# Optimization experiments

Measured on AMD Instinct MI355X. Metric: run time of the kernel, lower is better.

Reference implementation:

```python
import jax, jax.numpy as jnp
import numpy as np


def setup_inputs() -> dict:
    key = jax.random.key(0)
    k1, k2 = jax.random.split(key)
    x = jax.random.normal(k1, (16, 8192, 128), dtype=jnp.float32)
    embed = jax.random.normal(k2, (1024, 128), dtype=jnp.float32)
    return {"x": x, "embed": embed}


def reference(x, embed):
    # preprocess: flatten leading dims -> (N, d)
    shape = x.shape
    xf = x.reshape(-1, shape[-1])  # (N, d)
    # quantize: negative squared Euclidean distance, argmax over codebook
    dist = (2.0 * (xf @ embed.T)
            - jnp.sum(xf * xf, axis=1, keepdims=True)
            - jnp.sum(embed * embed, axis=1)[None, :])
    embed_ind = jnp.argmax(dist, axis=-1)  # (N,)
    # postprocess indices back to input leading shape
    embed_ind = embed_ind.reshape(shape[:-1])
    # dequantize: embedding lookup
    quantize = embed[embed_ind]  # (..., d)
    return embed_ind, quantize
```

## Files before the change

### kernel.cpp

```cpp
#include <hip/hip_runtime.h>
#include <math.h>


typedef __attribute__((ext_vector_type(8)))  short short8_t;
typedef __attribute__((ext_vector_type(16))) float floatx16;

constexpr int D        = 128;
constexpr int KCODES   = 1024;
constexpr int NTILES   = 32;
constexpr int ROWS_BLK = 128;
constexpr float TAU    = 0.015f;

constexpr size_t WS_NCSQ = 0;
constexpr size_t WS_EHI  = 4096;
constexpr size_t WS_ELO  = WS_EHI + 262144;
constexpr size_t WS_EMBT = WS_ELO + 262144;

#define GLOBAL_AS __attribute__((address_space(1)))
#define LDS_AS    __attribute__((address_space(3)))

__device__ inline unsigned short bf16_rne(float v, float* back) {
    unsigned u = __float_as_uint(v);
    unsigned r = (u + 0x7FFFu + ((u >> 16) & 1u)) >> 16;
    *back = __uint_as_float(r << 16);
    return (unsigned short)r;
}

__global__ __launch_bounds__(256)
void ecb_prep(const float* __restrict__ embed, float* __restrict__ ncsq,
              unsigned short* __restrict__ ehi, unsigned short* __restrict__ elo,
              float* __restrict__ embT) {
    const int tid = threadIdx.x;
    const int cc = tid & 15;
    const int nl = tid >> 4;
    const int n  = blockIdx.x * 16 + nl;
    const int t = n >> 5, nn = n & 31;
    const float* src = embed + (size_t)n * D + cc * 8;
    float4 a = *(const float4*)src;
    float4 b = *(const float4*)(src + 4);
    float vv[8] = {a.x, a.y, a.z, a.w, b.x, b.y, b.z, b.w};
    float ss = 0.f;
    unsigned short hq[8], lq[8];
#pragma unroll
    for (int j = 0; j < 8; ++j) {
        ss = fmaf(vv[j], vv[j], ss);
        float hb, db;
        hq[j] = bf16_rne(vv[j], &hb);
        lq[j] = bf16_rne(vv[j] - hb, &db);
    }
    uint4 ph, pl;
    ph.x = (unsigned)hq[0] | ((unsigned)hq[1] << 16);
    ph.y = (unsigned)hq[2] | ((unsigned)hq[3] << 16);
    ph.z = (unsigned)hq[4] | ((unsigned)hq[5] << 16);
    ph.w = (unsigned)hq[6] | ((unsigned)hq[7] << 16);
    pl.x = (unsigned)lq[0] | ((unsigned)lq[1] << 16);
    pl.y = (unsigned)lq[2] | ((unsigned)lq[3] << 16);
    pl.z = (unsigned)lq[4] | ((unsigned)lq[5] << 16);
    pl.w = (unsigned)lq[6] | ((unsigned)lq[7] << 16);
    size_t dst = ((size_t)(t * 8 + (cc >> 1)) * 64 + (size_t)((cc & 1) * 32 + nn)) * 8;
    *(uint4*)(ehi + dst) = ph;
    *(uint4*)(elo + dst) = pl;
#pragma unroll
    for (int j = 0; j < 8; ++j) embT[(size_t)(cc * 8 + j) * KCODES + n] = vv[j];
#pragma unroll
    for (int m = 1; m < 16; m <<= 1) ss += __shfl_xor(ss, m, 64);
    if (cc == 0) ncsq[n] = -ss;
}

__global__ __launch_bounds__(256, 3)
void ecb_main(const float* __restrict__ x,
              const unsigned short* __restrict__ ehi, const unsigned short* __restrict__ elo,
              const float* __restrict__ ncsq, const float* __restrict__ embed,
              const float* __restrict__ embT,
              float* __restrict__ out_idx, float* __restrict__ out_q) {
    __shared__ short8_t ebuf[2][2][512];
    __shared__ float ncsq_s[KCODES];
    __shared__ int   sidx[ROWS_BLK];
    __shared__ unsigned char llist[ROWS_BLK];
    __shared__ unsigned lcount;

    const int tid  = threadIdx.x;
    const int lane = tid & 63, wave = tid >> 6;
    const int col  = lane & 31, h = lane >> 5;
    const long rowblk = (long)blockIdx.x * ROWS_BLK;
    const int  roww   = wave * 32;

    if (tid == 0) lcount = 0u;
    ((float4*)ncsq_s)[tid] = ((const float4*)ncsq)[tid];

    short8_t ah[8], al[8];
    {
        const float* xr = x + (rowblk + roww + col) * (long)D + h * 8;
#pragma unroll
        for (int c = 0; c < 8; ++c) {
            float4 a  = *(const float4*)(xr + c * 16);
            float4 b  = *(const float4*)(xr + c * 16 + 4);
            float vv[8] = {a.x, a.y, a.z, a.w, b.x, b.y, b.z, b.w};
            short8_t fh, fl;
#pragma unroll
            for (int j = 0; j < 8; ++j) {
                float v2x = vv[j] + vv[j];
                float hb, db;
                fh[j] = (short)bf16_rne(v2x, &hb);
                fl[j] = (short)bf16_rne(v2x - hb, &db);
            }
            ah[c] = fh;
            al[c] = fl;
        }
    }

    auto stage = [&](int t, int bb) {
        const char* gh = (const char*)ehi + (size_t)t * 8192;
        const char* gl = (const char*)elo + (size_t)t * 8192;
        char* lh = (char*)&ebuf[bb][0][0];
        char* ll = (char*)&ebuf[bb][1][0];
        const int off = wave * 2048;
        __builtin_amdgcn_global_load_lds((const GLOBAL_AS unsigned int*)(gh + off + lane * 16),
                                         (LDS_AS unsigned int*)(lh + off), 16, 0, 0);
        __builtin_amdgcn_global_load_lds((const GLOBAL_AS unsigned int*)(gh + off + 1024 + lane * 16),
                                         (LDS_AS unsigned int*)(lh + off + 1024), 16, 0, 0);
        __builtin_amdgcn_global_load_lds((const GLOBAL_AS unsigned int*)(gl + off + lane * 16),
                                         (LDS_AS unsigned int*)(ll + off), 16, 0, 0);
        __builtin_amdgcn_global_load_lds((const GLOBAL_AS unsigned int*)(gl + off + 1024 + lane * 16),
                                         (LDS_AS unsigned int*)(ll + off + 1024), 16, 0, 0);
    };

    float v1[16], v2[16];
#pragma unroll
    for (int j = 0; j < 16; ++j) { v1[j] = -INFINITY; v2[j] = -INFINITY; }

    __syncthreads();
    stage(0, 0);

#pragma unroll 1
    for (int t = 0; t < NTILES; ++t) {
        const int b = t & 1;
        if (t + 1 < NTILES) {
            stage(t + 1, b ^ 1);
            asm volatile("s_waitcnt vmcnt(4)" ::: "memory");
        } else {
            asm volatile("s_waitcnt vmcnt(0)" ::: "memory");
        }
        __builtin_amdgcn_sched_barrier(0);
        __builtin_amdgcn_s_barrier();

        const float negcs = ncsq_s[t * 32 + col];
        floatx16 accA, accB;
#pragma unroll
        for (int i = 0; i < 16; ++i) { accA[i] = negcs; accB[i] = 0.f; }

        __builtin_amdgcn_s_setprio(1);
#pragma unroll
        for (int s = 0; s < 8; ++s) {
            short8_t bh = ebuf[b][0][s * 64 + lane];
            short8_t bl = ebuf[b][1][s * 64 + lane];
            accA = __builtin_amdgcn_mfma_f32_32x32x16_bf16(ah[s], bh, accA, 0, 0, 0);
            accB = __builtin_amdgcn_mfma_f32_32x32x16_bf16(al[s], bh, accB, 0, 0, 0);
            accB = __builtin_amdgcn_mfma_f32_32x32x16_bf16(ah[s], bl, accB, 0, 0, 0);
        }
        __builtin_amdgcn_s_setprio(0);

#pragma unroll
        for (int j = 0; j < 16; ++j) {
            float sc = accA[j] + accB[j];
            unsigned u = (__float_as_uint(sc) & ~31u) | (unsigned)t;
            float cand = __uint_as_float(u);
            float mn = fminf(v1[j], cand);
            v1[j] = fmaxf(v1[j], cand);
            v2[j] = fmaxf(v2[j], mn);
        }

        asm volatile("s_waitcnt lgkmcnt(0)" ::: "memory");
        __builtin_amdgcn_sched_barrier(0);
        __builtin_amdgcn_s_barrier();
    }

#pragma unroll
    for (int j = 0; j < 16; ++j) {
        float a1 = v1[j], a2 = v2[j];
        int   c1 = (int)((__float_as_uint(a1) & 31u) << 5) | col;
#pragma unroll
        for (int m = 1; m < 32; m <<= 1) {
            float o1 = __shfl_xor(a1, m, 64);
            int   oc = __shfl_xor(c1, m, 64);
            float o2 = __shfl_xor(a2, m, 64);
            float lo = fminf(a1, o1);
            if (o1 > a1) { a1 = o1; c1 = oc; }
            a2 = fmaxf(fmaxf(a2, o2), lo);
        }
        if (col == j) {
            int row_local = roww + (j & 3) + 8 * (j >> 2) + 4 * h;
            sidx[row_local] = c1;
            out_idx[rowblk + row_local] = (float)c1;
            if (a1 - a2 < TAU) {
                unsigned p = atomicAdd(&lcount, 1u);
                llist[p] = (unsigned char)row_local;
            }
        }
    }
    __syncthreads();

    for (int i = tid; i < ROWS_BLK * 32; i += 256) {
        int r = i >> 5, q = i & 31;
        int code = sidx[r];
        float4 ev = *(const float4*)(embed + (size_t)code * D + q * 4);
        *(float4*)(out_q + (rowblk + r) * (long)D + q * 4) = ev;
    }
    __syncthreads();

    float* xs = (float*)&ebuf[0][0][0];
    float* bv = xs + D;
    int*   bi = (int*)(bv + 256);
    const unsigned nf = lcount;
    const float4* eT = (const float4*)embT;
    for (unsigned f = 0; f < nf; ++f) {
        const int rl  = llist[f];
        const long row = rowblk + rl;
        if (tid < 32) *(float4*)&xs[tid * 4] = *(const float4*)(x + row * D + tid * 4);
        __syncthreads();
        float4 dot = {0.f, 0.f, 0.f, 0.f};
#pragma unroll 8
        for (int k = 0; k < D; ++k) {
            float xv = xs[k];
            float4 e = eT[(size_t)k * 256 + tid];
            dot.x = fmaf(xv, e.x, dot.x);
            dot.y = fmaf(xv, e.y, dot.y);
            dot.z = fmaf(xv, e.z, dot.z);
            dot.w = fmaf(xv, e.w, dot.w);
        }
        const int c0 = tid * 4;
        float scs[4] = {fmaf(2.f, dot.x, ncsq_s[c0]),
                        fmaf(2.f, dot.y, ncsq_s[c0 + 1]),
                        fmaf(2.f, dot.z, ncsq_s[c0 + 2]),
                        fmaf(2.f, dot.w, ncsq_s[c0 + 3])};
        float best = -INFINITY; int bidx = 0;
#pragma unroll
        for (int i = 0; i < 4; ++i)
            if (scs[i] > best) { best = scs[i]; bidx = c0 + i; }
        bv[tid] = best; bi[tid] = bidx;
        __syncthreads();
        for (int s = 128; s > 0; s >>= 1) {
            if (tid < s) {
                float ov = bv[tid + s]; int oi = bi[tid + s];
                if (ov > bv[tid] || (ov == bv[tid] && oi < bi[tid])) { bv[tid] = ov; bi[tid] = oi; }
            }
            __syncthreads();
        }
        const int win = bi[0];
        if (tid == 0) out_idx[row] = (float)win;
        if (tid < 32) {
            float4 ev = *(const float4*)(embed + (size_t)win * D + tid * 4);
            *(float4*)(out_q + row * D + tid * 4) = ev;
        }
        __syncthreads();
    }
}

extern "C" void kernel_launch(void* const* d_in, const int* in_sizes, int n_in,
                              void* d_out, int out_size, void* d_ws, size_t ws_size,
                              hipStream_t stream) {
    const float* x     = (const float*)d_in[0];
    const float* embed = (const float*)d_in[1];
    const int N = in_sizes[0] / D;
    char* ws = (char*)d_ws;
    float*          ncsq = (float*)(ws + WS_NCSQ);
    unsigned short* ehi  = (unsigned short*)(ws + WS_EHI);
    unsigned short* elo  = (unsigned short*)(ws + WS_ELO);
    float*          embT = (float*)(ws + WS_EMBT);
    float* out_idx = (float*)d_out;
    float* out_q   = out_idx + N;

    hipLaunchKernelGGL(ecb_prep, dim3(64), dim3(256), 0, stream,
                       embed, ncsq, ehi, elo, embT);
    hipLaunchKernelGGL(ecb_main, dim3(N / ROWS_BLK), dim3(256), 0, stream,
                       x, ehi, elo, ncsq, embed, embT, out_idx, out_q);
}
```

Baseline: 239.2 us.

## Process two 32-row groups per wave to reuse each codebook tile

Each wave now handles 64 rows (two 32-row MFMA groups), so every block covers 256 rows and each codebook tile staged in LDS serves twice as many MFMAs. The correction MFMAs accumulate into a single accumulator per group, removing the separate accB and the final add. The first tile's prefetch is issued before the x loads so the two overlap. In exchange the extra A fragments and running top-2 state raise register pressure, occupancy drops to 2 blocks per SM, and there are half as many blocks.

```diff
diff --git a/kernel.cpp b/kernel.cpp
--- a/kernel.cpp
+++ b/kernel.cpp
@@ -8,7 +8,7 @@
 constexpr int D        = 128;
 constexpr int KCODES   = 1024;
 constexpr int NTILES   = 32;
-constexpr int ROWS_BLK = 128;
+constexpr int ROWS_BLK = 256;
 constexpr float TAU    = 0.015f;
 
 constexpr size_t WS_NCSQ = 0;
@@ -24,6 +24,20 @@
     unsigned r = (u + 0x7FFFu + ((u >> 16) & 1u)) >> 16;
     *back = __uint_as_float(r << 16);
     return (unsigned short)r;
+}
+
+__device__ inline void cvt8x2(const float4 a, const float4 b,
+                              short8_t* fh, short8_t* fl) {
+    float vv[8] = {a.x, a.y, a.z, a.w, b.x, b.y, b.z, b.w};
+    short8_t h, l;
+#pragma unroll
+    for (int j = 0; j < 8; ++j) {
+        float v2x = vv[j] + vv[j];
+        float hb, db;
+        h[j] = (short)bf16_rne(v2x, &hb);
+        l[j] = (short)bf16_rne(v2x - hb, &db);
+    }
+    *fh = h; *fl = l;
 }
 
 __global__ __launch_bounds__(256)
@@ -67,7 +81,7 @@
     if (cc == 0) ncsq[n] = -ss;
 }
 
-__global__ __launch_bounds__(256, 3)
+__global__ __launch_bounds__(256, 2)
 void ecb_main(const float* __restrict__ x,
               const unsigned short* __restrict__ ehi, const unsigned short* __restrict__ elo,
               const float* __restrict__ ncsq, const float* __restrict__ embed,
@@ -83,31 +97,9 @@
     const int lane = tid & 63, wave = tid >> 6;
     const int col  = lane & 31, h = lane >> 5;
     const long rowblk = (long)blockIdx.x * ROWS_BLK;
-    const int  roww   = wave * 32;
+    const int  roww   = wave * 64;
 
     if (tid == 0) lcount = 0u;
-    ((float4*)ncsq_s)[tid] = ((const float4*)ncsq)[tid];
-
-    short8_t ah[8], al[8];
-    {
-        const float* xr = x + (rowblk + roww + col) * (long)D + h * 8;
-#pragma unroll
-        for (int c = 0; c < 8; ++c) {
-            float4 a  = *(const float4*)(xr + c * 16);
-            float4 b  = *(const float4*)(xr + c * 16 + 4);
-            float vv[8] = {a.x, a.y, a.z, a.w, b.x, b.y, b.z, b.w};
-            short8_t fh, fl;
-#pragma unroll
-            for (int j = 0; j < 8; ++j) {
-                float v2x = vv[j] + vv[j];
-                float hb, db;
-                fh[j] = (short)bf16_rne(v2x, &hb);
-                fl[j] = (short)bf16_rne(v2x - hb, &db);
-            }
-            ah[c] = fh;
-            al[c] = fl;
-        }
-    }
 
     auto stage = [&](int t, int bb) {
         const char* gh = (const char*)ehi + (size_t)t * 8192;
@@ -125,12 +117,32 @@
                                          (LDS_AS unsigned int*)(ll + off + 1024), 16, 0, 0);
     };
 
-    float v1[16], v2[16];
-#pragma unroll
-    for (int j = 0; j < 16; ++j) { v1[j] = -INFINITY; v2[j] = -INFINITY; }
-
-    __syncthreads();
     stage(0, 0);
+    ((float4*)ncsq_s)[tid] = ((const float4*)ncsq)[tid];
+
+    short8_t ah0[8], al0[8], ah1[8], al1[8];
+    {
+        const float* xr0 = x + (rowblk + roww + col) * (long)D + h * 8;
+        const float* xr1 = xr0 + 32 * (long)D;
+#pragma unroll
+        for (int c = 0; c < 8; ++c) {
+            cvt8x2(*(const float4*)(xr0 + c * 16), *(const float4*)(xr0 + c * 16 + 4),
+                   &ah0[c], &al0[c]);
+            cvt8x2(*(const float4*)(xr1 + c * 16), *(const float4*)(xr1 + c * 16 + 4),
+                   &ah1[c], &al1[c]);
+        }
+    }
+
+    float v1a[16], v2a[16], v1b[16], v2b[16];
+#pragma unroll
+    for (int j = 0; j < 16; ++j) {
+        v1a[j] = -INFINITY; v2a[j] = -INFINITY;
+        v1b[j] = -INFINITY; v2b[j] = -INFINITY;
+    }
+
+    asm volatile("s_waitcnt lgkmcnt(0)" ::: "memory");
+    __builtin_amdgcn_sched_barrier(0);
+    __builtin_amdgcn_s_barrier();
 
 #pragma unroll 1
     for (int t = 0; t < NTILES; ++t) {
@@ -145,29 +157,36 @@
         __builtin_amdgcn_s_barrier();
 
         const float negcs = ncsq_s[t * 32 + col];
-        floatx16 accA, accB;
-#pragma unroll
-        for (int i = 0; i < 16; ++i) { accA[i] = negcs; accB[i] = 0.f; }
+        floatx16 acc0, acc1;
+#pragma unroll
+        for (int i = 0; i < 16; ++i) { acc0[i] = negcs; acc1[i] = negcs; }
 
         __builtin_amdgcn_s_setprio(1);
 #pragma unroll
         for (int s = 0; s < 8; ++s) {
             short8_t bh = ebuf[b][0][s * 64 + lane];
             short8_t bl = ebuf[b][1][s * 64 + lane];
-            accA = __builtin_amdgcn_mfma_f32_32x32x16_bf16(ah[s], bh, accA, 0, 0, 0);
-            accB = __builtin_amdgcn_mfma_f32_32x32x16_bf16(al[s], bh, accB, 0, 0, 0);
-            accB = __builtin_amdgcn_mfma_f32_32x32x16_bf16(ah[s], bl, accB, 0, 0, 0);
+            acc0 = __builtin_amdgcn_mfma_f32_32x32x16_bf16(ah0[s], bl, acc0, 0, 0, 0);
+            acc1 = __builtin_amdgcn_mfma_f32_32x32x16_bf16(ah1[s], bl, acc1, 0, 0, 0);
+            acc0 = __builtin_amdgcn_mfma_f32_32x32x16_bf16(al0[s], bh, acc0, 0, 0, 0);
+            acc1 = __builtin_amdgcn_mfma_f32_32x32x16_bf16(al1[s], bh, acc1, 0, 0, 0);
+            acc0 = __builtin_amdgcn_mfma_f32_32x32x16_bf16(ah0[s], bh, acc0, 0, 0, 0);
+            acc1 = __builtin_amdgcn_mfma_f32_32x32x16_bf16(ah1[s], bh, acc1, 0, 0, 0);
         }
         __builtin_amdgcn_s_setprio(0);
 
 #pragma unroll
         for (int j = 0; j < 16; ++j) {
-            float sc = accA[j] + accB[j];
-            unsigned u = (__float_as_uint(sc) & ~31u) | (unsigned)t;
-            float cand = __uint_as_float(u);
-            float mn = fminf(v1[j], cand);
-            v1[j] = fmaxf(v1[j], cand);
-            v2[j] = fmaxf(v2[j], mn);
+            unsigned u0 = (__float_as_uint(acc0[j]) & ~31u) | (unsigned)t;
+            float cand0 = __uint_as_float(u0);
+            float mn0 = fminf(v1a[j], cand0);
+            v1a[j] = fmaxf(v1a[j], cand0);
+            v2a[j] = fmaxf(v2a[j], mn0);
+            unsigned u1 = (__float_as_uint(acc1[j]) & ~31u) | (unsigned)t;
+            float cand1 = __uint_as_float(u1);
+            float mn1 = fminf(v1b[j], cand1);
+            v1b[j] = fmaxf(v1b[j], cand1);
+            v2b[j] = fmaxf(v2b[j], mn1);
         }
 
         asm volatile("s_waitcnt lgkmcnt(0)" ::: "memory");
@@ -175,29 +194,33 @@
         __builtin_amdgcn_s_barrier();
     }
 
-#pragma unroll
-    for (int j = 0; j < 16; ++j) {
-        float a1 = v1[j], a2 = v2[j];
-        int   c1 = (int)((__float_as_uint(a1) & 31u) << 5) | col;
-#pragma unroll
-        for (int m = 1; m < 32; m <<= 1) {
-            float o1 = __shfl_xor(a1, m, 64);
-            int   oc = __shfl_xor(c1, m, 64);
-            float o2 = __shfl_xor(a2, m, 64);
-            float lo = fminf(a1, o1);
-            if (o1 > a1) { a1 = o1; c1 = oc; }
-            a2 = fmaxf(fmaxf(a2, o2), lo);
-        }
-        if (col == j) {
-            int row_local = roww + (j & 3) + 8 * (j >> 2) + 4 * h;
-            sidx[row_local] = c1;
-            out_idx[rowblk + row_local] = (float)c1;
-            if (a1 - a2 < TAU) {
-                unsigned p = atomicAdd(&lcount, 1u);
-                llist[p] = (unsigned char)row_local;
+    auto merge_group = [&](float* v1, float* v2, int gbase) {
+#pragma unroll
+        for (int j = 0; j < 16; ++j) {
+            float a1 = v1[j], a2 = v2[j];
+            int   c1 = (int)((__float_as_uint(a1) & 31u) << 5) | col;
+#pragma unroll
+            for (int m = 1; m < 32; m <<= 1) {
+                float o1 = __shfl_xor(a1, m, 64);
+                int   oc = __shfl_xor(c1, m, 64);
+                float o2 = __shfl_xor(a2, m, 64);
+                float lo = fminf(a1, o1);
+                if (o1 > a1) { a1 = o1; c1 = oc; }
+                a2 = fmaxf(fmaxf(a2, o2), lo);
             }
-        }
-    }
+            if (col == j) {
+                int row_local = gbase + (j & 3) + 8 * (j >> 2) + 4 * h;
+                sidx[row_local] = c1;
+                out_idx[rowblk + row_local] = (float)c1;
+                if (a1 - a2 < TAU) {
+                    unsigned p = atomicAdd(&lcount, 1u);
+                    llist[p] = (unsigned char)row_local;
+                }
+            }
+        }
+    };
+    merge_group(v1a, v2a, roww);
+    merge_group(v1b, v2b, roww + 32);
     __syncthreads();
 
     for (int i = tid; i < ROWS_BLK * 32; i += 256) {
```

Measured after the change: 257.6 us. +7.7%, slower.

## Drop codebook low-bf16 split, triple-buffer tiles, widen fp32 refinement threshold

Applied to the files above, without the earlier changes.

The codebook is now held only as high bf16 (no low residual), so each tile needs two MFMAs instead of three and loads half the codebook data. Staging moves to a three-slot LDS ring with a single barrier per tile, and the runner-up tracking uses fmed3. The margin threshold for exact fp32 re-checking rises from 0.015 to 0.25 to cover the larger bf16 error. More rows may now fall into the serial fp32 refinement path, and the occupancy hint drops from 3 to 2 blocks.

```diff
diff --git a/kernel.cpp b/kernel.cpp
--- a/kernel.cpp
+++ b/kernel.cpp
@@ -9,12 +9,11 @@
 constexpr int KCODES   = 1024;
 constexpr int NTILES   = 32;
 constexpr int ROWS_BLK = 128;
-constexpr float TAU    = 0.015f;
+constexpr float TAU    = 0.25f;
 
 constexpr size_t WS_NCSQ = 0;
 constexpr size_t WS_EHI  = 4096;
-constexpr size_t WS_ELO  = WS_EHI + 262144;
-constexpr size_t WS_EMBT = WS_ELO + 262144;
+constexpr size_t WS_EMBT = WS_EHI + 262144;
 
 #define GLOBAL_AS __attribute__((address_space(1)))
 #define LDS_AS    __attribute__((address_space(3)))
@@ -28,8 +27,7 @@
 
 __global__ __launch_bounds__(256)
 void ecb_prep(const float* __restrict__ embed, float* __restrict__ ncsq,
-              unsigned short* __restrict__ ehi, unsigned short* __restrict__ elo,
-              float* __restrict__ embT) {
+              unsigned short* __restrict__ ehi, float* __restrict__ embT) {
     const int tid = threadIdx.x;
     const int cc = tid & 15;
     const int nl = tid >> 4;
@@ -40,26 +38,20 @@
     float4 b = *(const float4*)(src + 4);
     float vv[8] = {a.x, a.y, a.z, a.w, b.x, b.y, b.z, b.w};
     float ss = 0.f;
-    unsigned short hq[8], lq[8];
+    unsigned short hq[8];
 #pragma unroll
     for (int j = 0; j < 8; ++j) {
         ss = fmaf(vv[j], vv[j], ss);
-        float hb, db;
+        float hb;
         hq[j] = bf16_rne(vv[j], &hb);
-        lq[j] = bf16_rne(vv[j] - hb, &db);
-    }
-    uint4 ph, pl;
+    }
+    uint4 ph;
     ph.x = (unsigned)hq[0] | ((unsigned)hq[1] << 16);
     ph.y = (unsigned)hq[2] | ((unsigned)hq[3] << 16);
     ph.z = (unsigned)hq[4] | ((unsigned)hq[5] << 16);
     ph.w = (unsigned)hq[6] | ((unsigned)hq[7] << 16);
-    pl.x = (unsigned)lq[0] | ((unsigned)lq[1] << 16);
-    pl.y = (unsigned)lq[2] | ((unsigned)lq[3] << 16);
-    pl.z = (unsigned)lq[4] | ((unsigned)lq[5] << 16);
-    pl.w = (unsigned)lq[6] | ((unsigned)lq[7] << 16);
     size_t dst = ((size_t)(t * 8 + (cc >> 1)) * 64 + (size_t)((cc & 1) * 32 + nn)) * 8;
     *(uint4*)(ehi + dst) = ph;
-    *(uint4*)(elo + dst) = pl;
 #pragma unroll
     for (int j = 0; j < 8; ++j) embT[(size_t)(cc * 8 + j) * KCODES + n] = vv[j];
 #pragma unroll
@@ -67,13 +59,13 @@
     if (cc == 0) ncsq[n] = -ss;
 }
 
-__global__ __launch_bounds__(256, 3)
+__global__ __launch_bounds__(256, 2)
 void ecb_main(const float* __restrict__ x,
-              const unsigned short* __restrict__ ehi, const unsigned short* __restrict__ elo,
+              const unsigned short* __restrict__ ehi,
               const float* __restrict__ ncsq, const float* __restrict__ embed,
               const float* __restrict__ embT,
               float* __restrict__ out_idx, float* __restrict__ out_q) {
-    __shared__ short8_t ebuf[2][2][512];
+    __shared__ short8_t ebuf[3][512];
     __shared__ float ncsq_s[KCODES];
     __shared__ int   sidx[ROWS_BLK];
     __shared__ unsigned char llist[ROWS_BLK];
@@ -86,6 +78,19 @@
     const int  roww   = wave * 32;
 
     if (tid == 0) lcount = 0u;
+
+    auto stage = [&](int t, int bs) {
+        const char* gh = (const char*)ehi + (size_t)t * 8192;
+        char* lh = (char*)&ebuf[bs][0];
+        const int off = wave * 2048;
+        __builtin_amdgcn_global_load_lds((const GLOBAL_AS unsigned int*)(gh + off + lane * 16),
+                                         (LDS_AS unsigned int*)(lh + off), 16, 0, 0);
+        __builtin_amdgcn_global_load_lds((const GLOBAL_AS unsigned int*)(gh + off + 1024 + lane * 16),
+                                         (LDS_AS unsigned int*)(lh + off + 1024), 16, 0, 0);
+    };
+
+    stage(0, 0);
+    stage(1, 1);
     ((float4*)ncsq_s)[tid] = ((const float4*)ncsq)[tid];
 
     short8_t ah[8], al[8];
@@ -109,70 +114,47 @@
         }
     }
 
-    auto stage = [&](int t, int bb) {
-        const char* gh = (const char*)ehi + (size_t)t * 8192;
-        const char* gl = (const char*)elo + (size_t)t * 8192;
-        char* lh = (char*)&ebuf[bb][0][0];
-        char* ll = (char*)&ebuf[bb][1][0];
-        const int off = wave * 2048;
-        __builtin_amdgcn_global_load_lds((const GLOBAL_AS unsigned int*)(gh + off + lane * 16),
-                                         (LDS_AS unsigned int*)(lh + off), 16, 0, 0);
-        __builtin_amdgcn_global_load_lds((const GLOBAL_AS unsigned int*)(gh + off + 1024 + lane * 16),
-                                         (LDS_AS unsigned int*)(lh + off + 1024), 16, 0, 0);
-        __builtin_amdgcn_global_load_lds((const GLOBAL_AS unsigned int*)(gl + off + lane * 16),
-                                         (LDS_AS unsigned int*)(ll + off), 16, 0, 0);
-        __builtin_amdgcn_global_load_lds((const GLOBAL_AS unsigned int*)(gl + off + 1024 + lane * 16),
-                                         (LDS_AS unsigned int*)(ll + off + 1024), 16, 0, 0);
-    };
-
     float v1[16], v2[16];
 #pragma unroll
     for (int j = 0; j < 16; ++j) { v1[j] = -INFINITY; v2[j] = -INFINITY; }
 
-    __syncthreads();
-    stage(0, 0);
+    asm volatile("s_waitcnt lgkmcnt(0)" ::: "memory");
+    __builtin_amdgcn_sched_barrier(0);
+    __builtin_amdgcn_s_barrier();
 
 #pragma unroll 1
     for (int t = 0; t < NTILES; ++t) {
-        const int b = t & 1;
-        if (t + 1 < NTILES) {
-            stage(t + 1, b ^ 1);
-            asm volatile("s_waitcnt vmcnt(4)" ::: "memory");
-        } else {
-            asm volatile("s_waitcnt vmcnt(0)" ::: "memory");
-        }
+        if (t + 1 < NTILES) asm volatile("s_waitcnt vmcnt(2)" ::: "memory");
+        else                asm volatile("s_waitcnt vmcnt(0)" ::: "memory");
         __builtin_amdgcn_sched_barrier(0);
         __builtin_amdgcn_s_barrier();
-
+        if (t + 2 < NTILES) stage(t + 2, (t + 2) % 3);
+
+        const int bs = t % 3;
         const float negcs = ncsq_s[t * 32 + col];
-        floatx16 accA, accB;
-#pragma unroll
-        for (int i = 0; i < 16; ++i) { accA[i] = negcs; accB[i] = 0.f; }
+
+        floatx16 acc;
+#pragma unroll
+        for (int i = 0; i < 16; ++i) acc[i] = 0.f;
 
         __builtin_amdgcn_s_setprio(1);
 #pragma unroll
         for (int s = 0; s < 8; ++s) {
-            short8_t bh = ebuf[b][0][s * 64 + lane];
-            short8_t bl = ebuf[b][1][s * 64 + lane];
-            accA = __builtin_amdgcn_mfma_f32_32x32x16_bf16(ah[s], bh, accA, 0, 0, 0);
-            accB = __builtin_amdgcn_mfma_f32_32x32x16_bf16(al[s], bh, accB, 0, 0, 0);
-            accB = __builtin_amdgcn_mfma_f32_32x32x16_bf16(ah[s], bl, accB, 0, 0, 0);
+            short8_t bh = ebuf[bs][s * 64 + lane];
+            acc = __builtin_amdgcn_mfma_f32_32x32x16_bf16(ah[s], bh, acc, 0, 0, 0);
+            acc = __builtin_amdgcn_mfma_f32_32x32x16_bf16(al[s], bh, acc, 0, 0, 0);
         }
         __builtin_amdgcn_s_setprio(0);
 
 #pragma unroll
         for (int j = 0; j < 16; ++j) {
-            float sc = accA[j] + accB[j];
+            float sc = acc[j] + negcs;
             unsigned u = (__float_as_uint(sc) & ~31u) | (unsigned)t;
             float cand = __uint_as_float(u);
-            float mn = fminf(v1[j], cand);
-            v1[j] = fmaxf(v1[j], cand);
-            v2[j] = fmaxf(v2[j], mn);
-        }
-
-        asm volatile("s_waitcnt lgkmcnt(0)" ::: "memory");
-        __builtin_amdgcn_sched_barrier(0);
-        __builtin_amdgcn_s_barrier();
+            float vo = v1[j];
+            v1[j] = fmaxf(vo, cand);
+            v2[j] = __builtin_amdgcn_fmed3f(vo, v2[j], cand);
+        }
     }
 
 #pragma unroll
@@ -208,7 +190,7 @@
     }
     __syncthreads();
 
-    float* xs = (float*)&ebuf[0][0][0];
+    float* xs = (float*)&ebuf[0][0];
     float* bv = xs + D;
     int*   bi = (int*)(bv + 256);
     const unsigned nf = lcount;
@@ -265,13 +247,12 @@
     char* ws = (char*)d_ws;
     float*          ncsq = (float*)(ws + WS_NCSQ);
     unsigned short* ehi  = (unsigned short*)(ws + WS_EHI);
-    unsigned short* elo  = (unsigned short*)(ws + WS_ELO);
     float*          embT = (float*)(ws + WS_EMBT);
     float* out_idx = (float*)d_out;
     float* out_q   = out_idx + N;
 
     hipLaunchKernelGGL(ecb_prep, dim3(64), dim3(256), 0, stream,
-                       embed, ncsq, ehi, elo, embT);
+                       embed, ncsq, ehi, embT);
     hipLaunchKernelGGL(ecb_main, dim3(N / ROWS_BLK), dim3(256), 0, stream,
-                       x, ehi, elo, ncsq, embed, embT, out_idx, out_q);
-}
+                       x, ehi, ncsq, embed, embT, out_idx, out_q);
+}
```

Result: slower. 291.9 us (+22.0%).

## Process codebook tiles in pairs per barrier and drop transposed embed copy

Applied to the files above, without the earlier changes.

The main loop now stages two 32-code tiles per step into a larger double buffer, which halves the number of block barriers. It replaces the explicit vmcnt waits with a single __syncthreads at the end of each pair. The top-2 update uses fmed3, and setprio is removed. The ambiguous-row fallback now reads the row-major embed directly instead of a transposed copy, so the prep kernel no longer writes embT. The doubled LDS buffer forces occupancy down from 3 to 2 blocks per CU, which may hurt latency hiding.

```diff
diff --git a/kernel.cpp b/kernel.cpp
--- a/kernel.cpp
+++ b/kernel.cpp
@@ -8,13 +8,13 @@
 constexpr int D        = 128;
 constexpr int KCODES   = 1024;
 constexpr int NTILES   = 32;
+constexpr int NPAIRS   = 16;
 constexpr int ROWS_BLK = 128;
 constexpr float TAU    = 0.015f;
 
 constexpr size_t WS_NCSQ = 0;
 constexpr size_t WS_EHI  = 4096;
 constexpr size_t WS_ELO  = WS_EHI + 262144;
-constexpr size_t WS_EMBT = WS_ELO + 262144;
 
 #define GLOBAL_AS __attribute__((address_space(1)))
 #define LDS_AS    __attribute__((address_space(3)))
@@ -28,8 +28,7 @@
 
 __global__ __launch_bounds__(256)
 void ecb_prep(const float* __restrict__ embed, float* __restrict__ ncsq,
-              unsigned short* __restrict__ ehi, unsigned short* __restrict__ elo,
-              float* __restrict__ embT) {
+              unsigned short* __restrict__ ehi, unsigned short* __restrict__ elo) {
     const int tid = threadIdx.x;
     const int cc = tid & 15;
     const int nl = tid >> 4;
@@ -61,19 +60,16 @@
     *(uint4*)(ehi + dst) = ph;
     *(uint4*)(elo + dst) = pl;
 #pragma unroll
-    for (int j = 0; j < 8; ++j) embT[(size_t)(cc * 8 + j) * KCODES + n] = vv[j];
-#pragma unroll
     for (int m = 1; m < 16; m <<= 1) ss += __shfl_xor(ss, m, 64);
     if (cc == 0) ncsq[n] = -ss;
 }
 
-__global__ __launch_bounds__(256, 3)
+__global__ __launch_bounds__(256, 2)
 void ecb_main(const float* __restrict__ x,
               const unsigned short* __restrict__ ehi, const unsigned short* __restrict__ elo,
               const float* __restrict__ ncsq, const float* __restrict__ embed,
-              const float* __restrict__ embT,
               float* __restrict__ out_idx, float* __restrict__ out_q) {
-    __shared__ short8_t ebuf[2][2][512];
+    __shared__ short8_t ebuf[2][2][2][512];
     __shared__ float ncsq_s[KCODES];
     __shared__ int   sidx[ROWS_BLK];
     __shared__ unsigned char llist[ROWS_BLK];
@@ -86,6 +82,27 @@
     const int  roww   = wave * 32;
 
     if (tid == 0) lcount = 0u;
+
+    auto stage = [&](int p, int bb) {
+#pragma unroll
+        for (int tt = 0; tt < 2; ++tt) {
+            const char* gh = (const char*)ehi + (size_t)(2 * p + tt) * 8192;
+            const char* gl = (const char*)elo + (size_t)(2 * p + tt) * 8192;
+            char* lh = (char*)&ebuf[bb][tt][0][0];
+            char* ll = (char*)&ebuf[bb][tt][1][0];
+            const int off = wave * 2048;
+            __builtin_amdgcn_global_load_lds((const GLOBAL_AS unsigned int*)(gh + off + lane * 16),
+                                             (LDS_AS unsigned int*)(lh + off), 16, 0, 0);
+            __builtin_amdgcn_global_load_lds((const GLOBAL_AS unsigned int*)(gh + off + 1024 + lane * 16),
+                                             (LDS_AS unsigned int*)(lh + off + 1024), 16, 0, 0);
+            __builtin_amdgcn_global_load_lds((const GLOBAL_AS unsigned int*)(gl + off + lane * 16),
+                                             (LDS_AS unsigned int*)(ll + off), 16, 0, 0);
+            __builtin_amdgcn_global_load_lds((const GLOBAL_AS unsigned int*)(gl + off + 1024 + lane * 16),
+                                             (LDS_AS unsigned int*)(ll + off + 1024), 16, 0, 0);
+        }
+    };
+
+    stage(0, 0);
     ((float4*)ncsq_s)[tid] = ((const float4*)ncsq)[tid];
 
     short8_t ah[8], al[8];
@@ -109,70 +126,46 @@
         }
     }
 
-    auto stage = [&](int t, int bb) {
-        const char* gh = (const char*)ehi + (size_t)t * 8192;
-        const char* gl = (const char*)elo + (size_t)t * 8192;
-        char* lh = (char*)&ebuf[bb][0][0];
-        char* ll = (char*)&ebuf[bb][1][0];
-        const int off = wave * 2048;
-        __builtin_amdgcn_global_load_lds((const GLOBAL_AS unsigned int*)(gh + off + lane * 16),
-                                         (LDS_AS unsigned int*)(lh + off), 16, 0, 0);
-        __builtin_amdgcn_global_load_lds((const GLOBAL_AS unsigned int*)(gh + off + 1024 + lane * 16),
-                                         (LDS_AS unsigned int*)(lh + off + 1024), 16, 0, 0);
-        __builtin_amdgcn_global_load_lds((const GLOBAL_AS unsigned int*)(gl + off + lane * 16),
-                                         (LDS_AS unsigned int*)(ll + off), 16, 0, 0);
-        __builtin_amdgcn_global_load_lds((const GLOBAL_AS unsigned int*)(gl + off + 1024 + lane * 16),
-                                         (LDS_AS unsigned int*)(ll + off + 1024), 16, 0, 0);
-    };
-
     float v1[16], v2[16];
 #pragma unroll
     for (int j = 0; j < 16; ++j) { v1[j] = -INFINITY; v2[j] = -INFINITY; }
 
     __syncthreads();
-    stage(0, 0);
 
 #pragma unroll 1
-    for (int t = 0; t < NTILES; ++t) {
-        const int b = t & 1;
-        if (t + 1 < NTILES) {
-            stage(t + 1, b ^ 1);
-            asm volatile("s_waitcnt vmcnt(4)" ::: "memory");
-        } else {
-            asm volatile("s_waitcnt vmcnt(0)" ::: "memory");
-        }
-        __builtin_amdgcn_sched_barrier(0);
-        __builtin_amdgcn_s_barrier();
-
-        const float negcs = ncsq_s[t * 32 + col];
-        floatx16 accA, accB;
-#pragma unroll
-        for (int i = 0; i < 16; ++i) { accA[i] = negcs; accB[i] = 0.f; }
-
-        __builtin_amdgcn_s_setprio(1);
-#pragma unroll
-        for (int s = 0; s < 8; ++s) {
-            short8_t bh = ebuf[b][0][s * 64 + lane];
-            short8_t bl = ebuf[b][1][s * 64 + lane];
-            accA = __builtin_amdgcn_mfma_f32_32x32x16_bf16(ah[s], bh, accA, 0, 0, 0);
-            accB = __builtin_amdgcn_mfma_f32_32x32x16_bf16(al[s], bh, accB, 0, 0, 0);
-            accB = __builtin_amdgcn_mfma_f32_32x32x16_bf16(ah[s], bl, accB, 0, 0, 0);
-        }
-        __builtin_amdgcn_s_setprio(0);
-
-#pragma unroll
-        for (int j = 0; j < 16; ++j) {
-            float sc = accA[j] + accB[j];
-            unsigned u = (__float_as_uint(sc) & ~31u) | (unsigned)t;
-            float cand = __uint_as_float(u);
-            float mn = fminf(v1[j], cand);
-            v1[j] = fmaxf(v1[j], cand);
-            v2[j] = fmaxf(v2[j], mn);
-        }
-
-        asm volatile("s_waitcnt lgkmcnt(0)" ::: "memory");
-        __builtin_amdgcn_sched_barrier(0);
-        __builtin_amdgcn_s_barrier();
+    for (int p = 0; p < NPAIRS; ++p) {
+        const int b = p & 1;
+        if (p + 1 < NPAIRS) stage(p + 1, b ^ 1);
+
+#pragma unroll
+        for (int tt = 0; tt < 2; ++tt) {
+            const int t = 2 * p + tt;
+            const float negcs = ncsq_s[t * 32 + col];
+
+            floatx16 accA, accB;
+#pragma unroll
+            for (int i = 0; i < 16; ++i) { accA[i] = negcs; accB[i] = 0.f; }
+
+#pragma unroll
+            for (int s = 0; s < 8; ++s) {
+                short8_t bh = ebuf[b][tt][0][s * 64 + lane];
+                short8_t bl = ebuf[b][tt][1][s * 64 + lane];
+                accA = __builtin_amdgcn_mfma_f32_32x32x16_bf16(ah[s], bh, accA, 0, 0, 0);
+                accB = __builtin_amdgcn_mfma_f32_32x32x16_bf16(al[s], bh, accB, 0, 0, 0);
+                accB = __builtin_amdgcn_mfma_f32_32x32x16_bf16(ah[s], bl, accB, 0, 0, 0);
+            }
+
+#pragma unroll
+            for (int j = 0; j < 16; ++j) {
+                float sc = accA[j] + accB[j];
+                unsigned u = (__float_as_uint(sc) & ~31u) | (unsigned)t;
+                float cand = __uint_as_float(u);
+                float vo = v1[j];
+                v1[j] = fmaxf(vo, cand);
+                v2[j] = __builtin_amdgcn_fmed3f(vo, v2[j], cand);
+            }
+        }
+        __syncthreads();
     }
 
 #pragma unroll
@@ -193,8 +186,8 @@
             sidx[row_local] = c1;
             out_idx[rowblk + row_local] = (float)c1;
             if (a1 - a2 < TAU) {
-                unsigned p = atomicAdd(&lcount, 1u);
-                llist[p] = (unsigned char)row_local;
+                unsigned p2 = atomicAdd(&lcount, 1u);
+                llist[p2] = (unsigned char)row_local;
             }
         }
     }
@@ -208,31 +201,37 @@
     }
     __syncthreads();
 
-    float* xs = (float*)&ebuf[0][0][0];
+    float* xs = (float*)&ebuf[0][0][0][0];
     float* bv = xs + D;
     int*   bi = (int*)(bv + 256);
     const unsigned nf = lcount;
-    const float4* eT = (const float4*)embT;
     for (unsigned f = 0; f < nf; ++f) {
         const int rl  = llist[f];
         const long row = rowblk + rl;
         if (tid < 32) *(float4*)&xs[tid * 4] = *(const float4*)(x + row * D + tid * 4);
         __syncthreads();
-        float4 dot = {0.f, 0.f, 0.f, 0.f};
-#pragma unroll 8
-        for (int k = 0; k < D; ++k) {
-            float xv = xs[k];
-            float4 e = eT[(size_t)k * 256 + tid];
-            dot.x = fmaf(xv, e.x, dot.x);
-            dot.y = fmaf(xv, e.y, dot.y);
-            dot.z = fmaf(xv, e.z, dot.z);
-            dot.w = fmaf(xv, e.w, dot.w);
-        }
         const int c0 = tid * 4;
-        float scs[4] = {fmaf(2.f, dot.x, ncsq_s[c0]),
-                        fmaf(2.f, dot.y, ncsq_s[c0 + 1]),
-                        fmaf(2.f, dot.z, ncsq_s[c0 + 2]),
-                        fmaf(2.f, dot.w, ncsq_s[c0 + 3])};
+        float s0 = 0.f, s1 = 0.f, s2 = 0.f, s3 = 0.f;
+#pragma unroll 4
+        for (int kc = 0; kc < 32; ++kc) {
+            float4 xv = *(const float4*)&xs[kc * 4];
+            float4 e0 = *(const float4*)(embed + (size_t)(c0 + 0) * D + kc * 4);
+            float4 e1 = *(const float4*)(embed + (size_t)(c0 + 1) * D + kc * 4);
+            float4 e2 = *(const float4*)(embed + (size_t)(c0 + 2) * D + kc * 4);
+            float4 e3 = *(const float4*)(embed + (size_t)(c0 + 3) * D + kc * 4);
+            s0 = fmaf(xv.x, e0.x, s0); s0 = fmaf(xv.y, e0.y, s0);
+            s0 = fmaf(xv.z, e0.z, s0); s0 = fmaf(xv.w, e0.w, s0);
+            s1 = fmaf(xv.x, e1.x, s1); s1 = fmaf(xv.y, e1.y, s1);
+            s1 = fmaf(xv.z, e1.z, s1); s1 = fmaf(xv.w, e1.w, s1);
+            s2 = fmaf(xv.x, e2.x, s2); s2 = fmaf(xv.y, e2.y, s2);
+            s2 = fmaf(xv.z, e2.z, s2); s2 = fmaf(xv.w, e2.w, s2);
+            s3 = fmaf(xv.x, e3.x, s3); s3 = fmaf(xv.y, e3.y, s3);
+            s3 = fmaf(xv.z, e3.z, s3); s3 = fmaf(xv.w, e3.w, s3);
+        }
+        float scs[4] = {fmaf(2.f, s0, ncsq_s[c0]),
+                        fmaf(2.f, s1, ncsq_s[c0 + 1]),
+                        fmaf(2.f, s2, ncsq_s[c0 + 2]),
+                        fmaf(2.f, s3, ncsq_s[c0 + 3])};
         float best = -INFINITY; int bidx = 0;
 #pragma unroll
         for (int i = 0; i < 4; ++i)
@@ -266,12 +265,11 @@
     float*          ncsq = (float*)(ws + WS_NCSQ);
     unsigned short* ehi  = (unsigned short*)(ws + WS_EHI);
     unsigned short* elo  = (unsigned short*)(ws + WS_ELO);
-    float*          embT = (float*)(ws + WS_EMBT);
     float* out_idx = (float*)d_out;
     float* out_q   = out_idx + N;
 
     hipLaunchKernelGGL(ecb_prep, dim3(64), dim3(256), 0, stream,
-                       embed, ncsq, ehi, elo, embT);
+                       embed, ncsq, ehi, elo);
     hipLaunchKernelGGL(ecb_main, dim3(N / ROWS_BLK), dim3(256), 0, stream,
-                       x, ehi, elo, ncsq, embed, embT, out_idx, out_q);
-}
+                       x, ehi, elo, ncsq, embed, out_idx, out_q);
+}
```

Result: slower. 281.9 us (+17.8%).
